# Performance work log

Hardware: AMD Instinct MI355X
Metric: run time of the kernel (lower is better)

Reference implementation:

```python
import jax, jax.numpy as jnp
import numpy as np

NQ = 10
C64 = jnp.complex64

# ---- gate matrices (built from traced fp32 params) ----

def u3(t, p, d):
    c = jnp.cos(t * 0.5).astype(C64)
    s = jnp.sin(t * 0.5).astype(C64)
    ep = jnp.exp(1j * p.astype(C64))
    ed = jnp.exp(1j * d.astype(C64))
    return jnp.stack([jnp.stack([c, -ed * s]), jnp.stack([ep * s, ep * ed * c])])

def ry(t):
    c = jnp.cos(t * 0.5).astype(C64)
    s = jnp.sin(t * 0.5).astype(C64)
    return jnp.stack([jnp.stack([c, -s]), jnp.stack([s, c])])

def rz(t):
    e = jnp.exp(-0.5j * t.astype(C64))
    ep = jnp.exp(0.5j * t.astype(C64))
    return jnp.diag(jnp.stack([e, ep]))

def rx(t):
    c = jnp.cos(t * 0.5).astype(C64)
    s = jnp.sin(t * 0.5).astype(C64)
    return jnp.stack([jnp.stack([c, -1j * s]), jnp.stack([-1j * s, c])])

def crz(t):
    one = jnp.ones((), C64)
    return jnp.diag(jnp.stack([one, one, jnp.exp(-0.5j * t.astype(C64)), jnp.exp(0.5j * t.astype(C64))]))

def crx(t):
    return jnp.eye(4, dtype=C64).at[2:, 2:].set(rx(t))

X = jnp.array([[0, 1], [1, 0]], dtype=C64)
CNOT = jnp.array([[1, 0, 0, 0], [0, 1, 0, 0], [0, 0, 0, 1], [0, 0, 1, 0]], dtype=C64)

# ---- gate application on state of shape (B, 2,...,2) ----

def ap1(st, U, w):
    ax = 1 + w
    s = jnp.moveaxis(st, ax, -1)
    s = s @ U.T
    return jnp.moveaxis(s, -1, ax)

def ap2(st, U, a, b):
    s = jnp.moveaxis(st, (1 + a, 1 + b), (-2, -1))
    sh = s.shape
    s = s.reshape(sh[:-2] + (4,)) @ U.T
    return jnp.moveaxis(s.reshape(sh), (-2, -1), (1 + a, 1 + b))

def conv_block(st, w, a, b):
    st = ap1(st, u3(w[0], w[1], w[2]), a)
    st = ap1(st, u3(w[3], w[4], w[5]), b)
    st = ap2(st, CNOT, a, b)
    st = ap1(st, ry(w[6]), a)
    st = ap1(st, rz(w[7]), b)
    st = ap2(st, CNOT, b, a)
    st = ap1(st, ry(w[8]), a)
    st = ap2(st, CNOT, a, b)
    st = ap1(st, u3(w[9], w[10], w[11]), a)
    st = ap1(st, u3(w[12], w[13], w[14]), b)
    return st

def pool_block(st, p, c, t):
    st = ap2(st, crz(p[0]), c, t)
    st = ap1(st, X, c)
    st = ap2(st, crx(p[1]), c, t)
    return st

def zexp(st, w):
    p = jnp.abs(st) ** 2  # fp32
    axes = tuple(ax for ax in range(1, NQ + 1) if ax != 1 + w)
    pz = p.sum(axis=axes)  # (B, 2)
    return pz[:, 0] - pz[:, 1]


def setup_inputs() -> dict:
    key = jax.random.key(0)
    ks = jax.random.split(key, 6)
    two_pi = 2.0 * np.pi
    return {
        "x": jax.random.normal(ks[0], (16384, 1024), dtype=jnp.float32),
        "weights_conv1": jax.random.uniform(ks[1], (10, 15), jnp.float32) * two_pi,
        "weights_conv2": jax.random.uniform(ks[2], (4, 15), jnp.float32) * two_pi,
        "weights_pool1": jax.random.uniform(ks[3], (5, 2), jnp.float32) * two_pi,
        "weights_pool2": jax.random.uniform(ks[4], (2, 2), jnp.float32) * two_pi,
        "weights_fc": jax.random.uniform(ks[5], (3,), jnp.float32) * two_pi,
    }


def reference(x, weights_conv1, weights_conv2, weights_pool1, weights_pool2, weights_fc):
    B = x.shape[0]
    # AmplitudeEmbedding with normalize=True (input already 1024-dim, no padding)
    nrm = jnp.linalg.norm(x, axis=1, keepdims=True)
    st = (x / nrm).astype(C64).reshape((B,) + (2,) * NQ)
    # conv layer 1: even pairs, odd pairs, wraparound (0, 9) reusing row 7
    for i in range(0, NQ, 2):
        st = conv_block(st, weights_conv1[i], i, i + 1)
    for i in range(1, NQ - 1, 2):
        st = conv_block(st, weights_conv1[i], i, i + 1)
    st = conv_block(st, weights_conv1[7], 0, NQ - 1)
    # pool layer 1
    for idx, i in enumerate(range(0, NQ, 2)):
        st = pool_block(st, weights_pool1[idx], i + 1, i)
    # conv layer 2 (stride-2 wires)
    for idx, i in enumerate(range(0, NQ - 2, 2)):
        st = conv_block(st, weights_conv2[idx], i, i + 2)
    # pool layer 2
    for idx, i in enumerate(range(0, NQ - 2, 4)):
        st = pool_block(st, weights_pool2[idx], i + 2, i)
    # fully-connected entanglers + RX rotations
    st = ap2(st, CNOT, 0, 4)
    st = ap2(st, CNOT, 2, 4)
    st = ap2(st, CNOT, 4, 0)
    st = ap1(st, rx(weights_fc[0]), 0)
    st = ap1(st, rx(weights_fc[1]), 2)
    st = ap1(st, rx(weights_fc[2]), 4)
    return jnp.stack([zexp(st, 0), zexp(st, 2)], axis=-1)  # (B, 2)
```

## Files before the change

### kernel.cpp

```cpp
#include <hip/hip_runtime.h>


typedef _Float16 f16;
typedef f16 f16x8 __attribute__((ext_vector_type(8)));
typedef f16 f16x4 __attribute__((ext_vector_type(4)));
typedef float f32x4 __attribute__((ext_vector_type(4)));

__device__ inline float2 cmul(float2 a, float2 b) {
    return make_float2(a.x * b.x - a.y * b.y, a.x * b.y + a.y * b.x);
}
__device__ inline float2 cadd(float2 a, float2 b) {
    return make_float2(a.x + b.x, a.y + b.y);
}

struct M2 { float2 m[4]; };

__device__ inline M2 m2_u3(float t, float p, float d) {
    float c = cosf(0.5f * t), s = sinf(0.5f * t);
    float2 ep = make_float2(cosf(p), sinf(p));
    float2 ed = make_float2(cosf(d), sinf(d));
    M2 U;
    U.m[0] = make_float2(c, 0.f);
    U.m[1] = make_float2(-ed.x * s, -ed.y * s);
    U.m[2] = make_float2(ep.x * s, ep.y * s);
    float2 epd = cmul(ep, ed);
    U.m[3] = make_float2(epd.x * c, epd.y * c);
    return U;
}
__device__ inline M2 m2_ry(float t) {
    float c = cosf(0.5f * t), s = sinf(0.5f * t);
    M2 U;
    U.m[0] = make_float2(c, 0.f);  U.m[1] = make_float2(-s, 0.f);
    U.m[2] = make_float2(s, 0.f);  U.m[3] = make_float2(c, 0.f);
    return U;
}
__device__ inline M2 m2_rz(float t) {
    float c = cosf(0.5f * t), s = sinf(0.5f * t);
    M2 U;
    U.m[0] = make_float2(c, -s); U.m[1] = make_float2(0.f, 0.f);
    U.m[2] = make_float2(0.f, 0.f); U.m[3] = make_float2(c, s);
    return U;
}
__device__ inline M2 m2_rx(float t) {
    float c = cosf(0.5f * t), s = sinf(0.5f * t);
    M2 U;
    U.m[0] = make_float2(c, 0.f);   U.m[1] = make_float2(0.f, -s);
    U.m[2] = make_float2(0.f, -s);  U.m[3] = make_float2(c, 0.f);
    return U;
}

__device__ inline void ap2x2(float2& x, float2& y, const M2& U) {
    float2 nx = cadd(cmul(U.m[0], x), cmul(U.m[1], y));
    float2 ny = cadd(cmul(U.m[2], x), cmul(U.m[3], y));
    x = nx; y = ny;
}
__device__ inline void apA(float2 v[4], const M2& U) { ap2x2(v[0], v[2], U); ap2x2(v[1], v[3], U); }
__device__ inline void apB(float2 v[4], const M2& U) { ap2x2(v[0], v[1], U); ap2x2(v[2], v[3], U); }
__device__ inline void swapv(float2& a, float2& b) { float2 t = a; a = b; b = t; }

__device__ inline void conv_col(const float* w, float2 v[4]) {
    apA(v, m2_u3(w[0], w[1], w[2]));
    apB(v, m2_u3(w[3], w[4], w[5]));
    swapv(v[2], v[3]);
    apA(v, m2_ry(w[6]));
    apB(v, m2_rz(w[7]));
    swapv(v[1], v[3]);
    apA(v, m2_ry(w[8]));
    swapv(v[2], v[3]);
    apA(v, m2_u3(w[9], w[10], w[11]));
    apB(v, m2_u3(w[12], w[13], w[14]));
}
__device__ inline void pool_col(const float* p, float2 v[4]) {
    {
        float c = cosf(0.5f * p[0]), s = sinf(0.5f * p[0]);
        v[2] = cmul(v[2], make_float2(c, -s));
        v[3] = cmul(v[3], make_float2(c, s));
    }
    swapv(v[0], v[2]); swapv(v[1], v[3]);
    {
        M2 U = m2_rx(p[1]);
        ap2x2(v[2], v[3], U);
    }
}

__global__ void build_gates(const float* wc1, const float* wc2,
                            const float* wp1, const float* wp2,
                            const float* wfc, int2* gp, float2* gm) {
    const int t = threadIdx.x;
    const int n = t >> 2, c = t & 3;
    if (blockIdx.x != 0 || n >= 27) return;

    float2 v[4];
    for (int i = 0; i < 4; i++) v[i] = make_float2(0.f, 0.f);
    v[c] = make_float2(1.f, 0.f);

    int a, b;
    if (n < 5)        { int i = 2*n;       a = i;   b = i+1; conv_col(wc1 + 15*i, v); }
    else if (n < 9)   { int i = 2*(n-5)+1; a = i;   b = i+1; conv_col(wc1 + 15*i, v); }
    else if (n == 9)  { a = 0; b = 9;      conv_col(wc1 + 105, v); }
    else if (n < 15)  { int idx = n-10, i = 2*idx; a = i+1; b = i; pool_col(wp1 + 2*idx, v); }
    else if (n < 19)  { int idx = n-15, i = 2*idx; a = i; b = i+2; conv_col(wc2 + 15*idx, v); }
    else if (n == 19) { a = 2; b = 0;      pool_col(wp2 + 0, v); }
    else if (n == 20) { a = 6; b = 4;      pool_col(wp2 + 2, v); }
    else if (n <= 23) {
        a = (n == 21) ? 0 : (n == 22) ? 2 : 4;
        b = (n == 23) ? 0 : 4;
        swapv(v[2], v[3]);
    } else {
        a = (n == 24) ? 0 : (n == 25) ? 2 : 4;
        b = a + 1;
        apA(v, m2_rx(wfc[n - 24]));
    }
    gp[n] = make_int2(9 - a, 9 - b);
    for (int i = 0; i < 4; i++) gm[n * 16 + i * 4 + c] = v[i];
}

__global__ __launch_bounds__(256) void build_U(const int2* __restrict__ gp,
                                               const float2* __restrict__ gm,
                                               float* __restrict__ B2) {
    __shared__ float2 st[2][1024];
    __shared__ float2 sm[27 * 16];
    const int t = blockIdx.x;
    for (int i = threadIdx.x; i < 27 * 16; i += 256) sm[i] = gm[i];
    for (int i = threadIdx.x; i < 1024; i += 256) st[0][i] = make_float2(0.f, 0.f);
    __syncthreads();
    if (threadIdx.x == 0) st[0][t] = make_float2(1.f, 0.f);
    __syncthreads();

    int cur = 0;
    for (int g = 0; g < 27; g++) {
        const int2 p = gp[g];
        const int p1 = p.x, p2 = p.y;
        const int lo = min(p1, p2), hi = max(p1, p2);
        const int q = threadIdx.x;
        const int m1 = (1 << lo) - 1;
        int tt = (q & m1) | ((q & ~m1) << 1);
        const int m2 = (1 << hi) - 1;
        const int i0 = (tt & m2) | ((tt & ~m2) << 1);
        int idx[4];
        for (int ga = 0; ga < 2; ga++)
            for (int gb = 0; gb < 2; gb++)
                idx[2 * ga + gb] = i0 | (ga << p1) | (gb << p2);
        float2 v[4];
        for (int i = 0; i < 4; i++) v[i] = st[cur][idx[i]];
        for (int i = 0; i < 4; i++) {
            float2 s = make_float2(0.f, 0.f);
            for (int j = 0; j < 4; j++) s = cadd(s, cmul(sm[g * 16 + i * 4 + j], v[j]));
            st[cur ^ 1][idx[i]] = s;
        }
        cur ^= 1;
        __syncthreads();
    }
    for (int s = threadIdx.x; s < 1024; s += 256) {
        const int b9 = (s >> 9) & 1, b7 = (s >> 7) & 1;
        if (b9 | b7) {
            const int grp = b9 ? b7 : 2;
            const int pos = (((s >> 8) & 1) << 7) | (s & 127);
            const int np = grp * 256 + pos;
            const float2 a = st[cur][s];
            B2[(size_t)t * 1536 + np] = a.x;
            B2[(size_t)t * 1536 + 768 + np] = a.y;
        }
    }
}

__global__ __launch_bounds__(256) void transpose_b(const float* __restrict__ B2,
                                                   f16* __restrict__ BTh) {
    __shared__ float t[32][33];
    const int n0 = blockIdx.x * 32, k0 = blockIdx.y * 32;
    const int c = threadIdx.x & 31, r = threadIdx.x >> 5;
#pragma unroll
    for (int i = 0; i < 4; i++) {
        int k = r + i * 8;
        t[k][c] = B2[(size_t)(k0 + k) * 1536 + n0 + c];
    }
    __syncthreads();
#pragma unroll
    for (int i = 0; i < 4; i++) {
        int n = r + i * 8;
        BTh[(size_t)(n0 + n) * 1024 + k0 + c] = (f16)t[c][n];
    }
}

__global__ __launch_bounds__(256) void norm_conv(const float* __restrict__ X,
                                                 float* __restrict__ nrm2,
                                                 f16* __restrict__ Xh) {
    const int b = blockIdx.x;
    float4 v = ((const float4*)(X + (size_t)b * 1024))[threadIdx.x];
    f16x4 h;
    h[0] = (f16)v.x; h[1] = (f16)v.y; h[2] = (f16)v.z; h[3] = (f16)v.w;
    *(f16x4*)(Xh + (size_t)b * 1024 + threadIdx.x * 4) = h;
    float s = v.x * v.x + v.y * v.y + v.z * v.z + v.w * v.w;
    for (int off = 32; off >= 1; off >>= 1) s += __shfl_xor(s, off, 64);
    __shared__ float ws2[4];
    const int lane = threadIdx.x & 63, wid = threadIdx.x >> 6;
    if (lane == 0) ws2[wid] = s;
    __syncthreads();
    if (threadIdx.x == 0) nrm2[b] = ws2[0] + ws2[1] + ws2[2] + ws2[3];
}

__device__ __forceinline__ void glds16(const void* g, void* l) {
    __builtin_amdgcn_global_load_lds(
        (const __attribute__((address_space(1))) void*)g,
        (__attribute__((address_space(3))) void*)l, 16, 0, 0);
}

__global__ __launch_bounds__(256) void gemm_mfma(const f16* __restrict__ A,
                                                 const f16* __restrict__ Bt,
                                                 float* __restrict__ partial) {
    __shared__ char Ash[8192];
    __shared__ char Bsh[8192];
    __shared__ float pLDS[128][2][2];
    const int tid = threadIdx.x;
    const int l = tid & 63, w = tid >> 6;
    const int wr = w >> 1, wc = w & 1;
    const int row0 = blockIdx.x * 128, col0 = blockIdx.y * 128;

    const int mrow = l >> 2;
    const int kc = (l & 3) ^ ((l >> 3) & 3);
    const f16* aS0 = A  + (size_t)(row0 + 32 * w + mrow) * 1024 + kc * 8;
    const f16* aS1 = aS0 + 16 * 1024;
    const f16* bS0 = Bt + (size_t)(col0 + 32 * w + mrow) * 1024 + kc * 8;
    const f16* bS1 = bS0 + 16 * 1024;
    char* aD0 = Ash + 2048 * w;
    char* aD1 = aD0 + 1024;
    char* bD0 = Bsh + 2048 * w;
    char* bD1 = bD0 + 1024;

    int aOff[4], bOff[4];
#pragma unroll
    for (int i = 0; i < 4; i++) {
        int m = wr * 64 + i * 16 + (l & 15);
        aOff[i] = m * 64 + (((l >> 4) ^ ((m >> 1) & 3)) << 4);
        int n = wc * 64 + i * 16 + (l & 15);
        bOff[i] = n * 64 + (((l >> 4) ^ ((n >> 1) & 3)) << 4);
    }

    f32x4 acc[4][4];
    const f32x4 z = {0.f, 0.f, 0.f, 0.f};
#pragma unroll
    for (int i = 0; i < 4; i++)
#pragma unroll
        for (int j = 0; j < 4; j++) acc[i][j] = z;

    for (int k0 = 0; k0 < 1024; k0 += 32) {
        glds16(aS0 + k0, aD0);
        glds16(aS1 + k0, aD1);
        glds16(bS0 + k0, bD0);
        glds16(bS1 + k0, bD1);
        __syncthreads();
        f16x8 af[4], bf[4];
#pragma unroll
        for (int i = 0; i < 4; i++) {
            af[i] = *(const f16x8*)(Ash + aOff[i]);
            bf[i] = *(const f16x8*)(Bsh + bOff[i]);
        }
#pragma unroll
        for (int mi = 0; mi < 4; mi++)
#pragma unroll
            for (int ni = 0; ni < 4; ni++)
                acc[mi][ni] = __builtin_amdgcn_mfma_f32_16x16x32_f16(
                    af[mi], bf[ni], acc[mi][ni], 0, 0, 0);
        __syncthreads();
    }

    float c0[4][4], c1[4][4];
#pragma unroll
    for (int mi = 0; mi < 4; mi++)
#pragma unroll
        for (int rr = 0; rr < 4; rr++) { c0[mi][rr] = 0.f; c1[mi][rr] = 0.f; }
#pragma unroll
    for (int ni = 0; ni < 4; ni++) {
        const int n_glob = col0 + wc * 64 + ni * 16 + (l & 15);
        const int nm = (n_glob >= 768) ? n_glob - 768 : n_glob;
        const int grp = nm >> 8;
        const float w0 = (grp <= 1) ? 1.f : 0.f;
        const float w1 = (grp >= 1) ? 1.f : 0.f;
#pragma unroll
        for (int mi = 0; mi < 4; mi++)
#pragma unroll
            for (int rr = 0; rr < 4; rr++) {
                const float y = acc[mi][ni][rr];
                const float y2 = y * y;
                c0[mi][rr] += w0 * y2;
                c1[mi][rr] += w1 * y2;
            }
    }
#pragma unroll
    for (int off = 1; off < 16; off <<= 1)
#pragma unroll
        for (int mi = 0; mi < 4; mi++)
#pragma unroll
            for (int rr = 0; rr < 4; rr++) {
                c0[mi][rr] += __shfl_xor(c0[mi][rr], off, 64);
                c1[mi][rr] += __shfl_xor(c1[mi][rr], off, 64);
            }
    if ((l & 15) == 0) {
        const int q = l >> 4;
#pragma unroll
        for (int mi = 0; mi < 4; mi++)
#pragma unroll
            for (int rr = 0; rr < 4; rr++) {
                const int r = wr * 64 + mi * 16 + q * 4 + rr;
                pLDS[r][wc][0] = c0[mi][rr];
                pLDS[r][wc][1] = c1[mi][rr];
            }
    }
    __syncthreads();
    {
        const int r = tid >> 1, k = tid & 1;
        const float v = pLDS[r][0][k] + pLDS[r][1][k];
        partial[((size_t)blockIdx.y * 16384 + row0 + r) * 2 + k] = v;
    }
}

__global__ __launch_bounds__(256) void finalize(const float* __restrict__ partial,
                                                const float* __restrict__ nrm2,
                                                float* __restrict__ out) {
    const int i = blockIdx.x * 256 + threadIdx.x;
    const int b = i >> 1, k = i & 1;
    float s = 0.f;
#pragma unroll
    for (int ny = 0; ny < 12; ny++) s += partial[((size_t)ny * 16384 + b) * 2 + k];
    out[i] = 1.f - 2.f * s / nrm2[b];
}

extern "C" void kernel_launch(void* const* d_in, const int* in_sizes, int n_in,
                              void* d_out, int out_size, void* d_ws, size_t ws_size,
                              hipStream_t stream) {
    const float* x   = (const float*)d_in[0];
    const float* wc1 = (const float*)d_in[1];
    const float* wc2 = (const float*)d_in[2];
    const float* wp1 = (const float*)d_in[3];
    const float* wp2 = (const float*)d_in[4];
    const float* wfc = (const float*)d_in[5];
    float* out = (float*)d_out;

    uintptr_t wsp = (uintptr_t)d_ws;
    int2*   gp     = (int2*)wsp;
    float2* gm     = (float2*)(wsp + 1024);
    float*  B2     = (float*)(wsp + 8192);
    f16*    BTh    = (f16*)(wsp + 8192 + (6u << 20));
    f16*    Xh     = (f16*)(wsp + 8192 + (9u << 20));
    float*  nrm2   = (float*)(wsp + 8192 + (41u << 20));
    float*  partial= (float*)(wsp + 8192 + (41u << 20) + 65536);

    build_gates<<<1, 128, 0, stream>>>(wc1, wc2, wp1, wp2, wfc, gp, gm);
    norm_conv<<<16384, 256, 0, stream>>>(x, nrm2, Xh);
    build_U<<<1024, 256, 0, stream>>>(gp, gm, B2);
    transpose_b<<<dim3(48, 32), 256, 0, stream>>>(B2, BTh);
    gemm_mfma<<<dim3(128, 12), 256, 0, stream>>>(Xh, BTh, partial);
    finalize<<<128, 256, 0, stream>>>(partial, nrm2, out);
}
```

Measured before the change: 229.1 us.

## Fuse gate building, unitary build, transpose and norm into one prep kernel

Merges build_gates, norm_conv, build_U and transpose_b into a single prep launch. The first 2048 blocks handle normalisation and fp16 conversion, eight rows per block with one wave per row. The remaining 1024 blocks each rebuild the gate matrices in shared memory and write the transposed fp16 B directly. This removes three launches, the fp32 B2 intermediate and the separate transpose pass. In exchange, every unitary block recomputes the gates redundantly, and the direct transposed stores are strided two-byte writes that will coalesce poorly.

```diff
diff --git a/kernel.cpp b/kernel.cpp
--- a/kernel.cpp
+++ b/kernel.cpp
@@ -83,60 +83,87 @@
     }
 }
 
-__global__ void build_gates(const float* wc1, const float* wc2,
-                            const float* wp1, const float* wp2,
-                            const float* wfc, int2* gp, float2* gm) {
-    const int t = threadIdx.x;
-    const int n = t >> 2, c = t & 3;
-    if (blockIdx.x != 0 || n >= 27) return;
-
-    float2 v[4];
-    for (int i = 0; i < 4; i++) v[i] = make_float2(0.f, 0.f);
-    v[c] = make_float2(1.f, 0.f);
-
-    int a, b;
-    if (n < 5)        { int i = 2*n;       a = i;   b = i+1; conv_col(wc1 + 15*i, v); }
-    else if (n < 9)   { int i = 2*(n-5)+1; a = i;   b = i+1; conv_col(wc1 + 15*i, v); }
-    else if (n == 9)  { a = 0; b = 9;      conv_col(wc1 + 105, v); }
-    else if (n < 15)  { int idx = n-10, i = 2*idx; a = i+1; b = i; pool_col(wp1 + 2*idx, v); }
-    else if (n < 19)  { int idx = n-15, i = 2*idx; a = i; b = i+2; conv_col(wc2 + 15*idx, v); }
-    else if (n == 19) { a = 2; b = 0;      pool_col(wp2 + 0, v); }
-    else if (n == 20) { a = 6; b = 4;      pool_col(wp2 + 2, v); }
-    else if (n <= 23) {
-        a = (n == 21) ? 0 : (n == 22) ? 2 : 4;
-        b = (n == 23) ? 0 : 4;
-        swapv(v[2], v[3]);
-    } else {
-        a = (n == 24) ? 0 : (n == 25) ? 2 : 4;
-        b = a + 1;
-        apA(v, m2_rx(wfc[n - 24]));
-    }
-    gp[n] = make_int2(9 - a, 9 - b);
-    for (int i = 0; i < 4; i++) gm[n * 16 + i * 4 + c] = v[i];
-}
-
-__global__ __launch_bounds__(256) void build_U(const int2* __restrict__ gp,
-                                               const float2* __restrict__ gm,
-                                               float* __restrict__ B2) {
+#define NORM_BLOCKS 2048
+
+__global__ __launch_bounds__(256) void prep(const float* __restrict__ X,
+                                            const float* __restrict__ wc1,
+                                            const float* __restrict__ wc2,
+                                            const float* __restrict__ wp1,
+                                            const float* __restrict__ wp2,
+                                            const float* __restrict__ wfc,
+                                            float* __restrict__ nrm2,
+                                            f16* __restrict__ Xh,
+                                            f16* __restrict__ BTh) {
     __shared__ float2 st[2][1024];
     __shared__ float2 sm[27 * 16];
-    const int t = blockIdx.x;
-    for (int i = threadIdx.x; i < 27 * 16; i += 256) sm[i] = gm[i];
-    for (int i = threadIdx.x; i < 1024; i += 256) st[0][i] = make_float2(0.f, 0.f);
-    __syncthreads();
-    if (threadIdx.x == 0) st[0][t] = make_float2(1.f, 0.f);
+    __shared__ int2 sgp[27];
+    const int bid = blockIdx.x;
+
+    if (bid < NORM_BLOCKS) {
+        const int w = threadIdx.x >> 6, l = threadIdx.x & 63;
+#pragma unroll
+        for (int r = 0; r < 2; r++) {
+            const int row = bid * 8 + w * 2 + r;
+            const float4* xr = (const float4*)(X + (size_t)row * 1024);
+            float s = 0.f;
+#pragma unroll
+            for (int ch = 0; ch < 4; ch++) {
+                float4 v = xr[ch * 64 + l];
+                f16x4 h;
+                h[0] = (f16)v.x; h[1] = (f16)v.y; h[2] = (f16)v.z; h[3] = (f16)v.w;
+                *(f16x4*)(Xh + (size_t)row * 1024 + (ch * 64 + l) * 4) = h;
+                s += v.x * v.x + v.y * v.y + v.z * v.z + v.w * v.w;
+            }
+#pragma unroll
+            for (int off = 32; off >= 1; off >>= 1) s += __shfl_xor(s, off, 64);
+            if (l == 0) nrm2[row] = s;
+        }
+        return;
+    }
+
+    const int t = bid - NORM_BLOCKS;
+
+    {
+        const int n = threadIdx.x >> 2, c = threadIdx.x & 3;
+        if (n < 27) {
+            float2 v[4];
+            for (int i = 0; i < 4; i++) v[i] = make_float2(0.f, 0.f);
+            v[c] = make_float2(1.f, 0.f);
+            int a, b;
+            if (n < 5)        { int i = 2*n;       a = i;   b = i+1; conv_col(wc1 + 15*i, v); }
+            else if (n < 9)   { int i = 2*(n-5)+1; a = i;   b = i+1; conv_col(wc1 + 15*i, v); }
+            else if (n == 9)  { a = 0; b = 9;      conv_col(wc1 + 105, v); }
+            else if (n < 15)  { int idx = n-10, i = 2*idx; a = i+1; b = i; pool_col(wp1 + 2*idx, v); }
+            else if (n < 19)  { int idx = n-15, i = 2*idx; a = i; b = i+2; conv_col(wc2 + 15*idx, v); }
+            else if (n == 19) { a = 2; b = 0;      pool_col(wp2 + 0, v); }
+            else if (n == 20) { a = 6; b = 4;      pool_col(wp2 + 2, v); }
+            else if (n <= 23) {
+                a = (n == 21) ? 0 : (n == 22) ? 2 : 4;
+                b = (n == 23) ? 0 : 4;
+                swapv(v[2], v[3]);
+            } else {
+                a = (n == 24) ? 0 : (n == 25) ? 2 : 4;
+                b = a + 1;
+                apA(v, m2_rx(wfc[n - 24]));
+            }
+            if (c == 0) sgp[n] = make_int2(9 - a, 9 - b);
+            for (int i = 0; i < 4; i++) sm[n * 16 + i * 4 + c] = v[i];
+        }
+    }
+    for (int i = threadIdx.x; i < 1024; i += 256)
+        st[0][i] = make_float2(i == t ? 1.f : 0.f, 0.f);
     __syncthreads();
 
     int cur = 0;
     for (int g = 0; g < 27; g++) {
-        const int2 p = gp[g];
+        const int2 p = sgp[g];
         const int p1 = p.x, p2 = p.y;
         const int lo = min(p1, p2), hi = max(p1, p2);
         const int q = threadIdx.x;
         const int m1 = (1 << lo) - 1;
         int tt = (q & m1) | ((q & ~m1) << 1);
-        const int m2 = (1 << hi) - 1;
-        const int i0 = (tt & m2) | ((tt & ~m2) << 1);
+        const int m2m = (1 << hi) - 1;
+        const int i0 = (tt & m2m) | ((tt & ~m2m) << 1);
         int idx[4];
         for (int ga = 0; ga < 2; ga++)
             for (int gb = 0; gb < 2; gb++)
@@ -151,6 +178,7 @@
         cur ^= 1;
         __syncthreads();
     }
+
     for (int s = threadIdx.x; s < 1024; s += 256) {
         const int b9 = (s >> 9) & 1, b7 = (s >> 7) & 1;
         if (b9 | b7) {
@@ -158,45 +186,10 @@
             const int pos = (((s >> 8) & 1) << 7) | (s & 127);
             const int np = grp * 256 + pos;
             const float2 a = st[cur][s];
-            B2[(size_t)t * 1536 + np] = a.x;
-            B2[(size_t)t * 1536 + 768 + np] = a.y;
-        }
-    }
-}
-
-__global__ __launch_bounds__(256) void transpose_b(const float* __restrict__ B2,
-                                                   f16* __restrict__ BTh) {
-    __shared__ float t[32][33];
-    const int n0 = blockIdx.x * 32, k0 = blockIdx.y * 32;
-    const int c = threadIdx.x & 31, r = threadIdx.x >> 5;
-#pragma unroll
-    for (int i = 0; i < 4; i++) {
-        int k = r + i * 8;
-        t[k][c] = B2[(size_t)(k0 + k) * 1536 + n0 + c];
-    }
-    __syncthreads();
-#pragma unroll
-    for (int i = 0; i < 4; i++) {
-        int n = r + i * 8;
-        BTh[(size_t)(n0 + n) * 1024 + k0 + c] = (f16)t[c][n];
-    }
-}
-
-__global__ __launch_bounds__(256) void norm_conv(const float* __restrict__ X,
-                                                 float* __restrict__ nrm2,
-                                                 f16* __restrict__ Xh) {
-    const int b = blockIdx.x;
-    float4 v = ((const float4*)(X + (size_t)b * 1024))[threadIdx.x];
-    f16x4 h;
-    h[0] = (f16)v.x; h[1] = (f16)v.y; h[2] = (f16)v.z; h[3] = (f16)v.w;
-    *(f16x4*)(Xh + (size_t)b * 1024 + threadIdx.x * 4) = h;
-    float s = v.x * v.x + v.y * v.y + v.z * v.z + v.w * v.w;
-    for (int off = 32; off >= 1; off >>= 1) s += __shfl_xor(s, off, 64);
-    __shared__ float ws2[4];
-    const int lane = threadIdx.x & 63, wid = threadIdx.x >> 6;
-    if (lane == 0) ws2[wid] = s;
-    __syncthreads();
-    if (threadIdx.x == 0) nrm2[b] = ws2[0] + ws2[1] + ws2[2] + ws2[3];
+            BTh[(size_t)np * 1024 + t] = (f16)a.x;
+            BTh[(size_t)(np + 768) * 1024 + t] = (f16)a.y;
+        }
+    }
 }
 
 __device__ __forceinline__ void glds16(const void* g, void* l) {
@@ -337,18 +330,12 @@
     float* out = (float*)d_out;
 
     uintptr_t wsp = (uintptr_t)d_ws;
-    int2*   gp     = (int2*)wsp;
-    float2* gm     = (float2*)(wsp + 1024);
-    float*  B2     = (float*)(wsp + 8192);
-    f16*    BTh    = (f16*)(wsp + 8192 + (6u << 20));
-    f16*    Xh     = (f16*)(wsp + 8192 + (9u << 20));
-    float*  nrm2   = (float*)(wsp + 8192 + (41u << 20));
-    float*  partial= (float*)(wsp + 8192 + (41u << 20) + 65536);
-
-    build_gates<<<1, 128, 0, stream>>>(wc1, wc2, wp1, wp2, wfc, gp, gm);
-    norm_conv<<<16384, 256, 0, stream>>>(x, nrm2, Xh);
-    build_U<<<1024, 256, 0, stream>>>(gp, gm, B2);
-    transpose_b<<<dim3(48, 32), 256, 0, stream>>>(B2, BTh);
+    f16*    BTh    = (f16*)wsp;
+    f16*    Xh     = (f16*)(wsp + (3u << 20));
+    float*  nrm2   = (float*)(wsp + (35u << 20));
+    float*  partial= (float*)(wsp + (35u << 20) + 65536);
+
+    prep<<<NORM_BLOCKS + 1024, 256, 0, stream>>>(x, wc1, wc2, wp1, wp2, wfc, nrm2, Xh, BTh);
     gemm_mfma<<<dim3(128, 12), 256, 0, stream>>>(Xh, BTh, partial);
     finalize<<<128, 256, 0, stream>>>(partial, nrm2, out);
 }
```

Result: slower. 233.9 us (+2.1%).
